# Optimization experiments

Hardware: AMD Instinct MI355X
Metric: run time of the kernel (lower is better)

## Reference

```python
import jax, jax.numpy as jnp
import numpy as np

NUM_HEADS = 8
IN_DIM = 384
HEAD_DIM = IN_DIM // NUM_HEADS  # 48


def setup_inputs() -> dict:
    key = jax.random.key(0)
    ks = jax.random.split(key, 6)
    B, N, M, C = 4, 4096, 1024, 384
    q_x = jax.random.normal(ks[0], (B, N, C), dtype=jnp.float32)
    kv_x = jax.random.normal(ks[1], (B, M, C), dtype=jnp.float32)
    s = C ** -0.5  # fan-in style init scale
    Wq = jax.random.normal(ks[2], (C, IN_DIM), dtype=jnp.float32) * s
    Wkv = jax.random.normal(ks[3], (C, 2 * IN_DIM), dtype=jnp.float32) * s
    Wproj = jax.random.normal(ks[4], (IN_DIM, IN_DIM), dtype=jnp.float32) * (IN_DIM ** -0.5)
    bproj = jnp.zeros((IN_DIM,), dtype=jnp.float32)
    return {"q_x": q_x, "kv_x": kv_x, "Wq": Wq, "Wkv": Wkv, "Wproj": Wproj, "bproj": bproj}


def reference(q_x, kv_x, Wq, Wkv, Wproj, bproj):
    B, N, C = q_x.shape
    M = kv_x.shape[1]
    scale = HEAD_DIM ** -0.5
    # q: [B, H, N, hd]
    q = (q_x @ Wq).reshape(B, N, NUM_HEADS, HEAD_DIM).transpose(0, 2, 1, 3)
    # k, v: [B, H, M, hd]
    kv = (kv_x @ Wkv).reshape(B, M, 2, NUM_HEADS, HEAD_DIM).transpose(2, 0, 3, 1, 4)
    k, v = kv[0], kv[1]
    # attention scores [B, H, N, M]
    attn = jax.nn.softmax(jnp.einsum('bhnd,bhmd->bhnm', q, k) * scale, axis=-1)
    x = jnp.einsum('bhnm,bhmd->bhnd', attn, v)  # [B, H, N, hd]
    x = x.transpose(0, 2, 1, 3).reshape(B, N, IN_DIM)
    x = x @ Wproj + bproj
    # sr_ratio == 1 residual: add raw q projection back
    q_res = q.transpose(0, 2, 1, 3).reshape(B, N, IN_DIM)
    return q_res + x
```

## Files before the change

kernel.cpp:

```cpp
#include <hip/hip_runtime.h>
#include <hip/hip_bf16.h>
#include <math.h>

#define B_ 4
#define N_ 4096
#define M_ 1024
#define C_ 384
#define NH_ 8
#define HD_ 48

typedef float f32x4 __attribute__((ext_vector_type(4)));
typedef short bf16x8 __attribute__((ext_vector_type(8)));

typedef __attribute__((address_space(3))) unsigned int lds_uint;
typedef const __attribute__((address_space(1))) unsigned int glob_uint;

__device__ __forceinline__ void gld_lds16(const void* g, void* l) {
    __builtin_amdgcn_global_load_lds((glob_uint*)g, (lds_uint*)l, 16, 0, 0);
}

__device__ __forceinline__ unsigned short f2bf(float x) {
    unsigned int u = __builtin_bit_cast(unsigned int, x);
    return (unsigned short)((u + 0x7FFFu + ((u >> 16) & 1u)) >> 16);
}
__device__ __forceinline__ unsigned short f2bf_trunc(float x) {
    return (unsigned short)(__builtin_bit_cast(unsigned int, x) >> 16);
}
__device__ __forceinline__ float bf2f(unsigned short x) {
    return __builtin_bit_cast(float, (unsigned int)x << 16);
}
__device__ __forceinline__ float fast_exp2(float x) {
#if __has_builtin(__builtin_amdgcn_exp2f)
    return __builtin_amdgcn_exp2f(x);
#else
    return exp2f(x);
#endif
}
__device__ __forceinline__ uint2 pack4_rne(float a, float b, float c, float d) {
    uint2 r;
    r.x = (unsigned int)f2bf(a) | ((unsigned int)f2bf(b) << 16);
    r.y = (unsigned int)f2bf(c) | ((unsigned int)f2bf(d) << 16);
    return r;
}

#define QSCALE 0.20823490983597203f

__global__ __launch_bounds__(256)
void prep(const float* __restrict__ qx_f, unsigned short* __restrict__ qx_bf,
          const float* __restrict__ kvx_f, unsigned short* __restrict__ kvx_bf,
          const float* __restrict__ Wq, const float* __restrict__ Wkv,
          const float* __restrict__ Wproj,
          unsigned short* __restrict__ Wq_t, unsigned short* __restrict__ Wkv_t,
          unsigned short* __restrict__ Wproj_t)
{
    __shared__ unsigned short T[64 * 72];
    const int tid = threadIdx.x;
    int bid = blockIdx.x;

    if (bid < 7680) {
        size_t i4 = (size_t)bid * 256 + tid;
        const float* src; unsigned short* dst;
        if (i4 < 1572864u) { src = qx_f; dst = qx_bf; }
        else { src = kvx_f; dst = kvx_bf; i4 -= 1572864u; }
        float4 v = *(const float4*)&src[i4 * 4];
        *(uint2*)&dst[i4 * 4] = pack4_rne(v.x, v.y, v.z, v.w);
        return;
    }

    bid -= 7680;
    const float* W; unsigned short* Wt; int N, kt, nt;
    if (bid < 36)       { W = Wq;    Wt = Wq_t;    N = 384; kt = bid / 6;  nt = bid - kt * 6; }
    else if (bid < 108) { bid -= 36;  W = Wkv;   Wt = Wkv_t;   N = 768; kt = bid / 12; nt = bid - kt * 12; }
    else                { bid -= 108; W = Wproj; Wt = Wproj_t; N = 384; kt = bid / 6;  nt = bid - kt * 6; }
    const int k0 = kt * 64, n0 = nt * 64;

    #pragma unroll
    for (int it = 0; it < 4; ++it) {
        int k = it * 16 + (tid >> 4);
        int n4 = (tid & 15) * 4;
        float4 v = *(const float4*)&W[(size_t)(k0 + k) * N + n0 + n4];
        T[(n4 + 0) * 72 + k] = f2bf(v.x);
        T[(n4 + 1) * 72 + k] = f2bf(v.y);
        T[(n4 + 2) * 72 + k] = f2bf(v.z);
        T[(n4 + 3) * 72 + k] = f2bf(v.w);
    }
    __syncthreads();
    #pragma unroll
    for (int i = 0; i < 2; ++i) {
        int s = tid + 256 * i;
        int n = s >> 3, part = s & 7;
        *(uint4*)&Wt[(size_t)(n0 + n) * C_ + k0 + part * 8] = *(const uint4*)&T[n * 72 + part * 8];
    }
}

__device__ __forceinline__ void stage128(const unsigned short* src, unsigned short* lds,
                                         int kk, int tid) {
    #pragma unroll
    for (int r = 0; r < 4; ++r) {
        int off = r * 256 + tid;
        int row = off >> 3;
        int c = off & 7;
        int gc = c ^ (row & 7);
        gld_lds16(src + (size_t)row * C_ + kk + gc * 8, lds + (size_t)off * 8);
    }
}
__device__ __forceinline__ bf16x8 frag_ld(const unsigned short* lds, int row, int chunk) {
    return *(const bf16x8*)&lds[row * 64 + ((chunk ^ (row & 7)) << 3)];
}

#define GEMM_CORE(Aptr, Wptr)                                                        \
    f32x4 acc[4][4];                                                                 \
    _Pragma("unroll")                                                                \
    for (int rt = 0; rt < 4; ++rt)                                                   \
        _Pragma("unroll")                                                            \
        for (int ct = 0; ct < 4; ++ct) acc[rt][ct] = (f32x4){0.f, 0.f, 0.f, 0.f};    \
    const int wrow0 = (wave & 1) * 64;                                               \
    const int wcol0 = (wave >> 1) * 64;                                              \
    for (int kk = 0; kk < C_; kk += 64) {                                            \
        __syncthreads();                                                             \
        stage128(Aptr, As, kk, tid);                                                 \
        stage128(Wptr, Ws, kk, tid);                                                 \
        __syncthreads();                                                             \
        _Pragma("unroll")                                                            \
        for (int ks = 0; ks < 2; ++ks) {                                             \
            bf16x8 af[4], wf[4];                                                     \
            _Pragma("unroll")                                                        \
            for (int rt = 0; rt < 4; ++rt)                                           \
                af[rt] = frag_ld(As, wrow0 + rt * 16 + ln, ks * 4 + quad);           \
            _Pragma("unroll")                                                        \
            for (int ct = 0; ct < 4; ++ct)                                           \
                wf[ct] = frag_ld(Ws, wcol0 + ct * 16 + ln, ks * 4 + quad);           \
            _Pragma("unroll")                                                        \
            for (int rt = 0; rt < 4; ++rt)                                           \
                _Pragma("unroll")                                                    \
                for (int ct = 0; ct < 4; ++ct)                                       \
                    acc[rt][ct] = __builtin_amdgcn_mfma_f32_16x16x32_bf16(           \
                        wf[ct], af[rt], acc[rt][ct], 0, 0, 0);                       \
        }                                                                            \
    }

__global__ __launch_bounds__(256)
void gemm_qkv(const unsigned short* __restrict__ qx, const unsigned short* __restrict__ kvx,
              const unsigned short* __restrict__ Wqt, const unsigned short* __restrict__ Wkvt,
              unsigned short* __restrict__ qbf, unsigned short* __restrict__ qres,
              unsigned short* __restrict__ kbf, unsigned short* __restrict__ vbf)
{
    __shared__ unsigned short As[128 * 64];
    __shared__ unsigned short Ws[128 * 64];
    const int tid = threadIdx.x;
    const int wave = tid >> 6;
    const int lane = tid & 63;
    const int ln = lane & 15;
    const int quad = lane >> 4;

    int bid = blockIdx.x;
    int mode, row0, col0;
    const unsigned short *A, *Wt;
    if (bid < 384) { mode = 0; A = qx;  Wt = Wqt;  row0 = (bid / 3) * 128; col0 = (bid % 3) * 128; }
    else { bid -= 384; mode = 1; A = kvx; Wt = Wkvt; row0 = (bid / 6) * 128; col0 = (bid % 6) * 128; }

    GEMM_CORE(A + (size_t)row0 * C_, Wt + (size_t)col0 * C_)

    #pragma unroll
    for (int rt = 0; rt < 4; ++rt) {
        int grow = row0 + wrow0 + rt * 16 + ln;
        #pragma unroll
        for (int ct = 0; ct < 4; ++ct) {
            int col = col0 + wcol0 + ct * 16 + quad * 4;
            f32x4 v = acc[rt][ct];
            if (mode == 0) {
                *(uint2*)&qres[(size_t)grow * C_ + col] = pack4_rne(v[0], v[1], v[2], v[3]);
                int b = grow >> 12, n = grow & (N_ - 1);
                int h = col / HD_, d = col - h * HD_;
                *(uint2*)&qbf[(((size_t)(b * NH_ + h) * N_) + n) * HD_ + d] =
                    pack4_rne(v[0] * QSCALE, v[1] * QSCALE, v[2] * QSCALE, v[3] * QSCALE);
            } else {
                int b = grow >> 10, m = grow & (M_ - 1);
                if (col < C_) {
                    int h = col / HD_, d = col - h * HD_;
                    *(uint2*)&kbf[(((size_t)(b * NH_ + h) * M_) + m) * HD_ + d] =
                        pack4_rne(v[0], v[1], v[2], v[3]);
                } else {
                    int c2 = col - C_;
                    int h = c2 / HD_, d = c2 - h * HD_;
                    size_t base = ((size_t)(b * NH_ + h) * HD_ + d) * M_ + m;
                    #pragma unroll
                    for (int r = 0; r < 4; ++r) vbf[base + (size_t)r * M_] = f2bf(v[r]);
                }
            }
        }
    }
}

__global__ __launch_bounds__(256)
void gemm_out(const unsigned short* __restrict__ A, const unsigned short* __restrict__ Wt,
              float* __restrict__ out0,
              const unsigned short* __restrict__ addend, const float* __restrict__ bias)
{
    __shared__ unsigned short As[128 * 64];
    __shared__ unsigned short Ws[128 * 64];
    const int tid = threadIdx.x;
    const int wave = tid >> 6;
    const int lane = tid & 63;
    const int ln = lane & 15;
    const int quad = lane >> 4;
    const int row0 = (blockIdx.x / 3) * 128;
    const int col0 = (blockIdx.x % 3) * 128;

    GEMM_CORE(A + (size_t)row0 * C_, Wt + (size_t)col0 * C_)

    #pragma unroll
    for (int rt = 0; rt < 4; ++rt) {
        int grow = row0 + wrow0 + rt * 16 + ln;
        #pragma unroll
        for (int ct = 0; ct < 4; ++ct) {
            int col = col0 + wcol0 + ct * 16 + quad * 4;
            f32x4 v = acc[rt][ct];
            size_t idx = (size_t)grow * C_ + col;
            uint2 ad = *(const uint2*)&addend[idx];
            float4 bi = *(const float4*)&bias[col];
            float4 o;
            o.x = v[0] + bf2f((unsigned short)(ad.x & 0xFFFF)) + bi.x;
            o.y = v[1] + bf2f((unsigned short)(ad.x >> 16))    + bi.y;
            o.z = v[2] + bf2f((unsigned short)(ad.y & 0xFFFF)) + bi.z;
            o.w = v[3] + bf2f((unsigned short)(ad.y >> 16))    + bi.w;
            *(float4*)&out0[idx] = o;
        }
    }
}

__global__ __launch_bounds__(256, 4)
void attn_mfma(const unsigned short* __restrict__ qbf,
               const unsigned short* __restrict__ kbf,
               const unsigned short* __restrict__ vbf,
               unsigned short* __restrict__ of)
{
    __shared__ unsigned short P[4][32 * 104];

    const int tid = threadIdx.x;
    const int wave = tid >> 6;
    const int lane = tid & 63;
    const int ln = lane & 15;
    const int quad = lane >> 4;
    const int bh = blockIdx.x;
    const int n0w = blockIdx.y * 128 + wave * 32;

    const bf16x8 zero8 = (bf16x8){0, 0, 0, 0, 0, 0, 0, 0};

    bf16x8 qb[2][2];
    #pragma unroll
    for (int qt = 0; qt < 2; ++qt) {
        const unsigned short* qp = qbf + ((size_t)bh * N_ + n0w + qt * 16 + ln) * HD_;
        qb[qt][0] = *(const bf16x8*)(qp + quad * 8);
        qb[qt][1] = *(const bf16x8*)(qp + 32 + quad * 8);
        if (quad >= 2) qb[qt][1] = zero8;
    }

    f32x4 O[3][2];
    #pragma unroll
    for (int ot = 0; ot < 3; ++ot)
        #pragma unroll
        for (int qt = 0; qt < 2; ++qt) O[ot][qt] = (f32x4){0.f, 0.f, 0.f, 0.f};
    float rs[2] = {0.f, 0.f};

    const unsigned short* kb = kbf + (size_t)bh * M_ * HD_;
    const unsigned short* vb = vbf + (size_t)bh * HD_ * M_;
    unsigned short* Pw = &P[wave][0];

    for (int mt = 0; mt < M_ / 64; ++mt) {
        bf16x8 va[3][2];
        #pragma unroll
        for (int ot = 0; ot < 3; ++ot) {
            const unsigned short* vp = vb + (size_t)(ot * 16 + ln) * M_ + mt * 64;
            va[ot][0] = *(const bf16x8*)(vp + quad * 8);
            va[ot][1] = *(const bf16x8*)(vp + 32 + quad * 8);
        }
        bf16x8 ka[4][2];
        #pragma unroll
        for (int t = 0; t < 4; ++t) {
            const unsigned short* kp = kb + (size_t)(mt * 64 + t * 16 + ln) * HD_;
            ka[t][0] = *(const bf16x8*)(kp + quad * 8);
            ka[t][1] = *(const bf16x8*)(kp + 32 + quad * 8);
            if (quad >= 2) ka[t][1] = zero8;
        }

        #pragma unroll
        for (int t = 0; t < 4; ++t) {
            #pragma unroll
            for (int qt = 0; qt < 2; ++qt) {
                f32x4 s = (f32x4){0.f, 0.f, 0.f, 0.f};
                s = __builtin_amdgcn_mfma_f32_16x16x32_bf16(ka[t][0], qb[qt][0], s, 0, 0, 0);
                s = __builtin_amdgcn_mfma_f32_16x16x32_bf16(ka[t][1], qb[qt][1], s, 0, 0, 0);
                float p0 = fast_exp2(s[0]);
                float p1 = fast_exp2(s[1]);
                float p2 = fast_exp2(s[2]);
                float p3 = fast_exp2(s[3]);
                rs[qt] += (p0 + p1) + (p2 + p3);
                uint2 pk;
                pk.x = (unsigned int)f2bf_trunc(p0) | ((unsigned int)f2bf_trunc(p1) << 16);
                pk.y = (unsigned int)f2bf_trunc(p2) | ((unsigned int)f2bf_trunc(p3) << 16);
                *(uint2*)&Pw[(qt * 16 + ln) * 104 + t * 16 + quad * 4] = pk;
            }
        }

        #pragma unroll
        for (int qt = 0; qt < 2; ++qt) {
            const unsigned short* Pr = &Pw[(qt * 16 + ln) * 104];
            bf16x8 pb0 = *(const bf16x8*)(Pr + quad * 8);
            bf16x8 pb1 = *(const bf16x8*)(Pr + 32 + quad * 8);
            #pragma unroll
            for (int ot = 0; ot < 3; ++ot) {
                O[ot][qt] = __builtin_amdgcn_mfma_f32_16x16x32_bf16(va[ot][0], pb0, O[ot][qt], 0, 0, 0);
                O[ot][qt] = __builtin_amdgcn_mfma_f32_16x16x32_bf16(va[ot][1], pb1, O[ot][qt], 0, 0, 0);
            }
        }
    }

    float inv[2];
    #pragma unroll
    for (int qt = 0; qt < 2; ++qt) {
        float x = rs[qt];
        x += __shfl_xor(x, 16);
        x += __shfl_xor(x, 32);
        inv[qt] = 1.0f / x;
    }

    const int b = bh >> 3, h = bh & 7;
    #pragma unroll
    for (int ot = 0; ot < 3; ++ot)
        #pragma unroll
        for (int qt = 0; qt < 2; ++qt) {
            size_t grow = (size_t)b * N_ + n0w + qt * 16 + ln;
            int gcol = h * HD_ + ot * 16 + quad * 4;
            *(uint2*)&of[grow * C_ + gcol] =
                pack4_rne(O[ot][qt][0] * inv[qt], O[ot][qt][1] * inv[qt],
                          O[ot][qt][2] * inv[qt], O[ot][qt][3] * inv[qt]);
        }
}

extern "C" void kernel_launch(void* const* d_in, const int* in_sizes, int n_in,
                              void* d_out, int out_size, void* d_ws, size_t ws_size,
                              hipStream_t stream) {
    const float* q_x   = (const float*)d_in[0];
    const float* kv_x  = (const float*)d_in[1];
    const float* Wq    = (const float*)d_in[2];
    const float* Wkv   = (const float*)d_in[3];
    const float* Wproj = (const float*)d_in[4];
    const float* bproj = (const float*)d_in[5];
    float* out = (float*)d_out;

    unsigned short* qbf     = (unsigned short*)d_ws;
    unsigned short* kbf     = qbf     + 6291456;
    unsigned short* vbf     = kbf     + 1572864;
    unsigned short* qres    = vbf     + 1572864;
    unsigned short* of      = qres    + 6291456;
    unsigned short* qx_bf   = of      + 6291456;
    unsigned short* kvx_bf  = qx_bf   + 6291456;
    unsigned short* Wq_t    = kvx_bf  + 1572864;
    unsigned short* Wkv_t   = Wq_t    + 147456;
    unsigned short* Wproj_t = Wkv_t   + 294912;

    dim3 blk(256);

    prep<<<dim3(7824), blk, 0, stream>>>(q_x, qx_bf, kv_x, kvx_bf,
                                         Wq, Wkv, Wproj, Wq_t, Wkv_t, Wproj_t);

    gemm_qkv<<<dim3(576), blk, 0, stream>>>(
        qx_bf, kvx_bf, Wq_t, Wkv_t, qbf, qres, kbf, vbf);

    attn_mfma<<<dim3(32, 32), blk, 0, stream>>>(qbf, kbf, vbf, of);

    gemm_out<<<dim3(384), blk, 0, stream>>>(of, Wproj_t, out, qres, bproj);
}
```

Measured before the change: 193.5 us.

## Use 32x32 MFMA in attention with register P shuffle; drop qres buffer

The attention kernel moves from 16x16x32 to 32x32x16 bf16 MFMA tiles, with 64 query rows per wave. It also drops the LDS staging of P and repacks probabilities between lanes with cross-half shuffles, which removes the zero-padded head-dim work and the LDS round trip. Separately, the residual qres buffer is no longer written: the output GEMM reads the scaled q tensor and multiplies by the inverse scale, saving one bf16 write pass. The cost is higher register pressure (occupancy bound lowered to 2), a strided residual read, and a small extra rounding error on the residual path.

```diff
diff --git a/kernel.cpp b/kernel.cpp
--- a/kernel.cpp
+++ b/kernel.cpp
@@ -10,6 +10,7 @@
 #define HD_ 48
 
 typedef float f32x4 __attribute__((ext_vector_type(4)));
+typedef float f32x16 __attribute__((ext_vector_type(16)));
 typedef short bf16x8 __attribute__((ext_vector_type(8)));
 
 typedef __attribute__((address_space(3))) unsigned int lds_uint;
@@ -22,9 +23,6 @@
 __device__ __forceinline__ unsigned short f2bf(float x) {
     unsigned int u = __builtin_bit_cast(unsigned int, x);
     return (unsigned short)((u + 0x7FFFu + ((u >> 16) & 1u)) >> 16);
-}
-__device__ __forceinline__ unsigned short f2bf_trunc(float x) {
-    return (unsigned short)(__builtin_bit_cast(unsigned int, x) >> 16);
 }
 __device__ __forceinline__ float bf2f(unsigned short x) {
     return __builtin_bit_cast(float, (unsigned int)x << 16);
@@ -44,6 +42,7 @@
 }
 
 #define QSCALE 0.20823490983597203f
+#define INV_QSCALE (1.0f / 0.20823490983597203f)
 
 __global__ __launch_bounds__(256)
 void prep(const float* __restrict__ qx_f, unsigned short* __restrict__ qx_bf,
@@ -142,7 +141,7 @@
 __global__ __launch_bounds__(256)
 void gemm_qkv(const unsigned short* __restrict__ qx, const unsigned short* __restrict__ kvx,
               const unsigned short* __restrict__ Wqt, const unsigned short* __restrict__ Wkvt,
-              unsigned short* __restrict__ qbf, unsigned short* __restrict__ qres,
+              unsigned short* __restrict__ qbf,
               unsigned short* __restrict__ kbf, unsigned short* __restrict__ vbf)
 {
     __shared__ unsigned short As[128 * 64];
@@ -169,7 +168,6 @@
             int col = col0 + wcol0 + ct * 16 + quad * 4;
             f32x4 v = acc[rt][ct];
             if (mode == 0) {
-                *(uint2*)&qres[(size_t)grow * C_ + col] = pack4_rne(v[0], v[1], v[2], v[3]);
                 int b = grow >> 12, n = grow & (N_ - 1);
                 int h = col / HD_, d = col - h * HD_;
                 *(uint2*)&qbf[(((size_t)(b * NH_ + h) * N_) + n) * HD_ + d] =
@@ -195,7 +193,7 @@
 __global__ __launch_bounds__(256)
 void gemm_out(const unsigned short* __restrict__ A, const unsigned short* __restrict__ Wt,
               float* __restrict__ out0,
-              const unsigned short* __restrict__ addend, const float* __restrict__ bias)
+              const unsigned short* __restrict__ qbf, const float* __restrict__ bias)
 {
     __shared__ unsigned short As[128 * 64];
     __shared__ unsigned short Ws[128 * 64];
@@ -217,125 +215,144 @@
             int col = col0 + wcol0 + ct * 16 + quad * 4;
             f32x4 v = acc[rt][ct];
             size_t idx = (size_t)grow * C_ + col;
-            uint2 ad = *(const uint2*)&addend[idx];
+            int b = grow >> 12, n = grow & (N_ - 1);
+            int h = col / HD_, d = col - h * HD_;
+            uint2 ad = *(const uint2*)&qbf[(((size_t)(b * NH_ + h) * N_) + n) * HD_ + d];
             float4 bi = *(const float4*)&bias[col];
             float4 o;
-            o.x = v[0] + bf2f((unsigned short)(ad.x & 0xFFFF)) + bi.x;
-            o.y = v[1] + bf2f((unsigned short)(ad.x >> 16))    + bi.y;
-            o.z = v[2] + bf2f((unsigned short)(ad.y & 0xFFFF)) + bi.z;
-            o.w = v[3] + bf2f((unsigned short)(ad.y >> 16))    + bi.w;
+            o.x = v[0] + bf2f((unsigned short)(ad.x & 0xFFFF)) * INV_QSCALE + bi.x;
+            o.y = v[1] + bf2f((unsigned short)(ad.x >> 16))    * INV_QSCALE + bi.y;
+            o.z = v[2] + bf2f((unsigned short)(ad.y & 0xFFFF)) * INV_QSCALE + bi.z;
+            o.w = v[3] + bf2f((unsigned short)(ad.y >> 16))    * INV_QSCALE + bi.w;
             *(float4*)&out0[idx] = o;
         }
     }
 }
 
-__global__ __launch_bounds__(256, 4)
+__global__ __launch_bounds__(256, 2)
 void attn_mfma(const unsigned short* __restrict__ qbf,
                const unsigned short* __restrict__ kbf,
                const unsigned short* __restrict__ vbf,
                unsigned short* __restrict__ of)
 {
-    __shared__ unsigned short P[4][32 * 104];
-
     const int tid = threadIdx.x;
     const int wave = tid >> 6;
     const int lane = tid & 63;
-    const int ln = lane & 15;
-    const int quad = lane >> 4;
+    const int l31 = lane & 31;
+    const int hi  = lane >> 5;
     const int bh = blockIdx.x;
-    const int n0w = blockIdx.y * 128 + wave * 32;
-
-    const bf16x8 zero8 = (bf16x8){0, 0, 0, 0, 0, 0, 0, 0};
-
-    bf16x8 qb[2][2];
-    #pragma unroll
-    for (int qt = 0; qt < 2; ++qt) {
-        const unsigned short* qp = qbf + ((size_t)bh * N_ + n0w + qt * 16 + ln) * HD_;
-        qb[qt][0] = *(const bf16x8*)(qp + quad * 8);
-        qb[qt][1] = *(const bf16x8*)(qp + 32 + quad * 8);
-        if (quad >= 2) qb[qt][1] = zero8;
-    }
-
-    f32x4 O[3][2];
-    #pragma unroll
-    for (int ot = 0; ot < 3; ++ot)
-        #pragma unroll
-        for (int qt = 0; qt < 2; ++qt) O[ot][qt] = (f32x4){0.f, 0.f, 0.f, 0.f};
-    float rs[2] = {0.f, 0.f};
+    const int n0w = blockIdx.y * 256 + wave * 64;
 
     const unsigned short* kb = kbf + (size_t)bh * M_ * HD_;
     const unsigned short* vb = vbf + (size_t)bh * HD_ * M_;
-    unsigned short* Pw = &P[wave][0];
-
-    for (int mt = 0; mt < M_ / 64; ++mt) {
-        bf16x8 va[3][2];
-        #pragma unroll
-        for (int ot = 0; ot < 3; ++ot) {
-            const unsigned short* vp = vb + (size_t)(ot * 16 + ln) * M_ + mt * 64;
-            va[ot][0] = *(const bf16x8*)(vp + quad * 8);
-            va[ot][1] = *(const bf16x8*)(vp + 32 + quad * 8);
+
+    bf16x8 qb[2][3];
+    #pragma unroll
+    for (int qt = 0; qt < 2; ++qt) {
+        const unsigned short* qp = qbf + ((size_t)bh * N_ + n0w + qt * 32 + l31) * HD_;
+        #pragma unroll
+        for (int s = 0; s < 3; ++s)
+            qb[qt][s] = *(const bf16x8*)(qp + s * 16 + hi * 8);
+    }
+
+    f32x16 O[2][2];
+    #pragma unroll
+    for (int qt = 0; qt < 2; ++qt)
+        #pragma unroll
+        for (int ot2 = 0; ot2 < 2; ++ot2)
+            #pragma unroll
+            for (int r = 0; r < 16; ++r) O[qt][ot2][r] = 0.f;
+    float rs[2] = {0.f, 0.f};
+
+    for (int mtt = 0; mtt < 32; ++mtt) {
+        const int m0 = mtt * 32;
+
+        bf16x8 ka[3];
+        #pragma unroll
+        for (int s = 0; s < 3; ++s)
+            ka[s] = *(const bf16x8*)&kb[(size_t)(m0 + l31) * HD_ + s * 16 + hi * 8];
+
+        bf16x8 va[2][2];
+        #pragma unroll
+        for (int ot2 = 0; ot2 < 2; ++ot2)
+            #pragma unroll
+            for (int s2 = 0; s2 < 2; ++s2)
+                va[ot2][s2] = *(const bf16x8*)&vb[(size_t)(ot2 * 32 + l31) * M_ + m0 + s2 * 16 + hi * 8];
+
+        #pragma unroll
+        for (int qt = 0; qt < 2; ++qt) {
+            f32x16 S;
+            #pragma unroll
+            for (int r = 0; r < 16; ++r) S[r] = 0.f;
+            #pragma unroll
+            for (int s = 0; s < 3; ++s)
+                S = __builtin_amdgcn_mfma_f32_32x32x16_bf16(ka[s], qb[qt][s], S, 0, 0, 0);
+
+            float p[16];
+            #pragma unroll
+            for (int r = 0; r < 16; ++r) p[r] = fast_exp2(S[r]);
+            {
+                float s0 = (p[0] + p[1]) + (p[2] + p[3]);
+                float s1 = (p[4] + p[5]) + (p[6] + p[7]);
+                float s2 = (p[8] + p[9]) + (p[10] + p[11]);
+                float s3 = (p[12] + p[13]) + (p[14] + p[15]);
+                rs[qt] += (s0 + s1) + (s2 + s3);
+            }
+
+            unsigned c0[4], c1[4];
+            #pragma unroll
+            for (int g = 0; g < 4; ++g) {
+                c0[g] = (__builtin_bit_cast(unsigned int, p[4 * g + 0]) >> 16) |
+                        (__builtin_bit_cast(unsigned int, p[4 * g + 1]) & 0xFFFF0000u);
+                c1[g] = (__builtin_bit_cast(unsigned int, p[4 * g + 2]) >> 16) |
+                        (__builtin_bit_cast(unsigned int, p[4 * g + 3]) & 0xFFFF0000u);
+            }
+
+            #pragma unroll
+            for (int s2 = 0; s2 < 2; ++s2) {
+                unsigned o00 = c0[2 * s2], o01 = c0[2 * s2 + 1];
+                unsigned o10 = c1[2 * s2], o11 = c1[2 * s2 + 1];
+                unsigned pr0 = (unsigned)__shfl_xor((int)(hi ? o00 : o01), 32);
+                unsigned pr1 = (unsigned)__shfl_xor((int)(hi ? o10 : o11), 32);
+                unsigned d0 = hi ? pr0 : o00;
+                unsigned d1 = hi ? pr1 : o10;
+                unsigned d2 = hi ? o01 : pr0;
+                unsigned d3 = hi ? o11 : pr1;
+                uint4 u = {d0, d1, d2, d3};
+                bf16x8 pf = __builtin_bit_cast(bf16x8, u);
+                #pragma unroll
+                for (int ot2 = 0; ot2 < 2; ++ot2)
+                    O[qt][ot2] = __builtin_amdgcn_mfma_f32_32x32x16_bf16(
+                        va[ot2][s2], pf, O[qt][ot2], 0, 0, 0);
+            }
         }
-        bf16x8 ka[4][2];
-        #pragma unroll
-        for (int t = 0; t < 4; ++t) {
-            const unsigned short* kp = kb + (size_t)(mt * 64 + t * 16 + ln) * HD_;
-            ka[t][0] = *(const bf16x8*)(kp + quad * 8);
-            ka[t][1] = *(const bf16x8*)(kp + 32 + quad * 8);
-            if (quad >= 2) ka[t][1] = zero8;
+    }
+
+    float inv[2];
+    #pragma unroll
+    for (int qt = 0; qt < 2; ++qt) {
+        float x = rs[qt] + __shfl_xor(rs[qt], 32);
+        inv[qt] = 1.0f / x;
+    }
+
+    const int b = bh >> 3, h = bh & 7;
+    #pragma unroll
+    for (int qt = 0; qt < 2; ++qt) {
+        size_t grow = (size_t)b * N_ + n0w + qt * 32 + l31;
+        unsigned short* orow = of + grow * C_ + h * HD_;
+        #pragma unroll
+        for (int ot2 = 0; ot2 < 2; ++ot2) {
+            const int rgmax = (ot2 == 0) ? 4 : 2;
+            #pragma unroll
+            for (int rg = 0; rg < 4; ++rg) {
+                if (rg >= rgmax) continue;
+                int d0 = ot2 * 32 + rg * 8 + hi * 4;
+                *(uint2*)(orow + d0) = pack4_rne(
+                    O[qt][ot2][rg * 4 + 0] * inv[qt], O[qt][ot2][rg * 4 + 1] * inv[qt],
+                    O[qt][ot2][rg * 4 + 2] * inv[qt], O[qt][ot2][rg * 4 + 3] * inv[qt]);
+            }
         }
-
-        #pragma unroll
-        for (int t = 0; t < 4; ++t) {
-            #pragma unroll
-            for (int qt = 0; qt < 2; ++qt) {
-                f32x4 s = (f32x4){0.f, 0.f, 0.f, 0.f};
-                s = __builtin_amdgcn_mfma_f32_16x16x32_bf16(ka[t][0], qb[qt][0], s, 0, 0, 0);
-                s = __builtin_amdgcn_mfma_f32_16x16x32_bf16(ka[t][1], qb[qt][1], s, 0, 0, 0);
-                float p0 = fast_exp2(s[0]);
-                float p1 = fast_exp2(s[1]);
-                float p2 = fast_exp2(s[2]);
-                float p3 = fast_exp2(s[3]);
-                rs[qt] += (p0 + p1) + (p2 + p3);
-                uint2 pk;
-                pk.x = (unsigned int)f2bf_trunc(p0) | ((unsigned int)f2bf_trunc(p1) << 16);
-                pk.y = (unsigned int)f2bf_trunc(p2) | ((unsigned int)f2bf_trunc(p3) << 16);
-                *(uint2*)&Pw[(qt * 16 + ln) * 104 + t * 16 + quad * 4] = pk;
-            }
-        }
-
-        #pragma unroll
-        for (int qt = 0; qt < 2; ++qt) {
-            const unsigned short* Pr = &Pw[(qt * 16 + ln) * 104];
-            bf16x8 pb0 = *(const bf16x8*)(Pr + quad * 8);
-            bf16x8 pb1 = *(const bf16x8*)(Pr + 32 + quad * 8);
-            #pragma unroll
-            for (int ot = 0; ot < 3; ++ot) {
-                O[ot][qt] = __builtin_amdgcn_mfma_f32_16x16x32_bf16(va[ot][0], pb0, O[ot][qt], 0, 0, 0);
-                O[ot][qt] = __builtin_amdgcn_mfma_f32_16x16x32_bf16(va[ot][1], pb1, O[ot][qt], 0, 0, 0);
-            }
-        }
-    }
-
-    float inv[2];
-    #pragma unroll
-    for (int qt = 0; qt < 2; ++qt) {
-        float x = rs[qt];
-        x += __shfl_xor(x, 16);
-        x += __shfl_xor(x, 32);
-        inv[qt] = 1.0f / x;
-    }
-
-    const int b = bh >> 3, h = bh & 7;
-    #pragma unroll
-    for (int ot = 0; ot < 3; ++ot)
-        #pragma unroll
-        for (int qt = 0; qt < 2; ++qt) {
-            size_t grow = (size_t)b * N_ + n0w + qt * 16 + ln;
-            int gcol = h * HD_ + ot * 16 + quad * 4;
-            *(uint2*)&of[grow * C_ + gcol] =
-                pack4_rne(O[ot][qt][0] * inv[qt], O[ot][qt][1] * inv[qt],
-                          O[ot][qt][2] * inv[qt], O[ot][qt][3] * inv[qt]);
-        }
+    }
 }
 
 extern "C" void kernel_launch(void* const* d_in, const int* in_sizes, int n_in,
@@ -352,8 +369,7 @@
     unsigned short* qbf     = (unsigned short*)d_ws;
     unsigned short* kbf     = qbf     + 6291456;
     unsigned short* vbf     = kbf     + 1572864;
-    unsigned short* qres    = vbf     + 1572864;
-    unsigned short* of      = qres    + 6291456;
+    unsigned short* of      = vbf     + 1572864;
     unsigned short* qx_bf   = of      + 6291456;
     unsigned short* kvx_bf  = qx_bf   + 6291456;
     unsigned short* Wq_t    = kvx_bf  + 1572864;
@@ -366,9 +382,9 @@
                                          Wq, Wkv, Wproj, Wq_t, Wkv_t, Wproj_t);
 
     gemm_qkv<<<dim3(576), blk, 0, stream>>>(
-        qx_bf, kvx_bf, Wq_t, Wkv_t, qbf, qres, kbf, vbf);
-
-    attn_mfma<<<dim3(32, 32), blk, 0, stream>>>(qbf, kbf, vbf, of);
-
-    gemm_out<<<dim3(384), blk, 0, stream>>>(of, Wproj_t, out, qres, bproj);
-}
+        qx_bf, kvx_bf, Wq_t, Wkv_t, qbf, kbf, vbf);
+
+    attn_mfma<<<dim3(32, 16), blk, 0, stream>>>(qbf, kbf, vbf, of);
+
+    gemm_out<<<dim3(384), blk, 0, stream>>>(of, Wproj_t, out, qbf, bproj);
+}
```

Result: faster. 168.8 us (-12.8%).
